# Kernel tuning notes

Hardware: AMD Instinct MI355X
Metric: run time of the kernel (lower is better)

## Reference

```python
import jax, jax.numpy as jnp
import numpy as np

N0, N1, N2, N3 = 524288, 262144, 65536, 8192
E0, E1, E2 = 2621440, 655360, 81920
D_IN, D_H, D_OUT = 256, 256, 64


def setup_inputs() -> dict:
    key = jax.random.key(0)
    ks = jax.random.split(key, 16)
    s = 0.02
    inp = {
        "x": jax.random.normal(ks[0], (N0, D_IN), dtype=jnp.float32),
        "src0": jax.random.randint(ks[1], (E0,), 0, N0, dtype=jnp.int32),
        "dst0": jax.random.randint(ks[2], (E0,), 0, N1, dtype=jnp.int32),
        "src1": jax.random.randint(ks[3], (E1,), 0, N1, dtype=jnp.int32),
        "dst1": jax.random.randint(ks[4], (E1,), 0, N2, dtype=jnp.int32),
        "src2": jax.random.randint(ks[5], (E2,), 0, N2, dtype=jnp.int32),
        "dst2": jax.random.randint(ks[6], (E2,), 0, N3, dtype=jnp.int32),
        "nd0": N1, "nd1": N2, "nd2": N3,
        "Wfc": jax.random.normal(ks[7], (D_IN, D_H), dtype=jnp.float32) * s,
        "bfc": jnp.zeros((D_H,), dtype=jnp.float32),
        "Ws0": jax.random.normal(ks[8], (D_H, D_H), dtype=jnp.float32) * s,
        "Wn0": jax.random.normal(ks[9], (D_H, D_H), dtype=jnp.float32) * s,
        "b0": jnp.zeros((D_H,), dtype=jnp.float32),
        "Ws1": jax.random.normal(ks[10], (D_H, D_H), dtype=jnp.float32) * s,
        "Wn1": jax.random.normal(ks[11], (D_H, D_H), dtype=jnp.float32) * s,
        "b1": jnp.zeros((D_H,), dtype=jnp.float32),
        "Ws2": jax.random.normal(ks[12], (D_H, D_OUT), dtype=jnp.float32) * s,
        "Wn2": jax.random.normal(ks[13], (D_H, D_OUT), dtype=jnp.float32) * s,
        "b2": jnp.zeros((D_OUT,), dtype=jnp.float32),
    }
    return inp


def sage_conv(h, src, dst, n_dst, Ws, Wn, b):
    # DGL SAGEConv 'mean': out = h_dst @ W_self + mean_neigh(h_src) @ W_neigh + b
    h_dst = h[:n_dst]
    msg = jnp.take(h, src, axis=0)                    # [E, d] gather
    agg = jax.ops.segment_sum(msg, dst, num_segments=n_dst)
    cnt = jax.ops.segment_sum(jnp.ones((dst.shape[0],), h.dtype), dst, num_segments=n_dst)
    mean = agg / jnp.maximum(cnt, 1.0)[:, None]
    return h_dst @ Ws + mean @ Wn + b


def reference(x, src0, dst0, src1, dst1, src2, dst2, nd0, nd1, nd2,
              Wfc, bfc, Ws0, Wn0, b0, Ws1, Wn1, b1, Ws2, Wn2, b2):
    h = jax.nn.relu(x @ Wfc + bfc)                    # input projection (dropout=0 -> identity)
    h = jax.nn.relu(sage_conv(h, src0, dst0, nd0, Ws0, Wn0, b0))
    h = jax.nn.relu(sage_conv(h, src1, dst1, nd1, Ws1, Wn1, b1))
    h = sage_conv(h, src2, dst2, nd2, Ws2, Wn2, b2)   # no activation on final layer
    return h
```

## Files before the change

kernel.cpp:

```cpp
#include <hip/hip_runtime.h>

constexpr int N0c = 524288, N1c = 262144, N2c = 65536, N3c = 8192;

typedef __attribute__((ext_vector_type(8))) short   bf16x8;
typedef __attribute__((ext_vector_type(4))) float   f32x4;
typedef __attribute__((ext_vector_type(4))) unsigned short u16x4;

__device__ inline unsigned short f2bf(float f) {
    union { float f; unsigned u; } v; v.f = f;
    unsigned r = v.u + 0x7FFF + ((v.u >> 16) & 1);
    return (unsigned short)(r >> 16);
}
__device__ inline float bf2f(unsigned short u) {
    union { unsigned u; float f; } v; v.u = ((unsigned)u) << 16;
    return v.f;
}

__device__ inline void glds16(const void* g, void* l) {
    __builtin_amdgcn_global_load_lds(
        (const __attribute__((address_space(1))) unsigned int*)g,
        (__attribute__((address_space(3))) unsigned int*)l, 16, 0, 0);
}

__global__ __launch_bounds__(256)
void wconv_k(const float* __restrict__ W, unsigned short* __restrict__ Wt, int K, int N)
{
    const int i = blockIdx.x * 256 + threadIdx.x;
    if (i >= K * N) return;
    const int k = i / N, n = i % N;
    Wt[n * K + k] = f2bf(W[i]);
}

__device__ inline bf16x8 pack_bf8(const float* p) {
    const f32x4 u = *(const f32x4*)p;
    const f32x4 v = *(const f32x4*)(p + 4);
    bf16x8 t;
    #pragma unroll
    for (int j = 0; j < 4; ++j) {
        t[j]     = (short)f2bf(u[j]);
        t[j + 4] = (short)f2bf(v[j]);
    }
    return t;
}

template<int NT, int KC, bool DUAL, bool RELU, bool A_F32, bool OUT_BF16>
__global__ __launch_bounds__(512, 2)
void gemm2(const void* __restrict__ A1v, const void* __restrict__ A2v,
           const unsigned short* __restrict__ Wt1,
           const unsigned short* __restrict__ Wt2,
           const float* __restrict__ bias, void* __restrict__ Cv)
{
    constexpr int N     = NT * 16;
    constexpr int PH    = 256 / KC;
    constexpr int SLOTS = KC / 8;
    constexpr int GPM   = N * SLOTS;
    constexpr int TOTG  = GPM * (DUAL ? 2 : 1);
    static_assert(TOTG == 4096, "LDS sizing");
    __shared__ unsigned short Bs[TOTG * 8];

    const int t    = threadIdx.x;
    const int lane = t & 63;
    const int wv   = t >> 6;
    const int col  = lane & 15;
    const int kg   = lane >> 4;
    const int swz  = (col & 7) << 3;
    const long row0 = (long)blockIdx.x * 128 + wv * 16;

    const unsigned short* A1h = (const unsigned short*)A1v;
    const float*          A1f = (const float*)A1v;
    const unsigned short* A2h = (const unsigned short*)A2v;

    f32x4 acc[NT];
    #pragma unroll
    for (int nt = 0; nt < NT; ++nt) acc[nt] = (f32x4){0.f, 0.f, 0.f, 0.f};

    const long ar = (row0 + col) * 256;

    for (int kh = 0; kh < PH; ++kh) {
        if (kh) __syncthreads();
        #pragma unroll
        for (int it = 0; it < TOTG / 512; ++it) {
            const int g  = it * 512 + t;
            const int m  = DUAL ? (g / GPM) : 0;
            const int gm = DUAL ? (g % GPM) : g;
            const int n  = gm / SLOTS;
            const int s  = gm % SLOTS;
            const int ss = s ^ (n & 7);
            const unsigned short* srcb =
                (m ? Wt2 : Wt1) + n * 256 + kh * KC + ss * 8;
            glds16(srcb, &Bs[(it * 512 + wv * 64) * 8]);
        }
        __syncthreads();

        #pragma unroll
        for (int k0 = 0; k0 < KC; k0 += 32) {
            const int kx = (k0 + kg * 8) ^ swz;
            const long ac = ar + kh * KC + k0 + kg * 8;
            bf16x8 a1, a2;
            if constexpr (A_F32) a1 = pack_bf8(&A1f[ac]);
            else                 a1 = *(const bf16x8*)&A1h[ac];
            if constexpr (DUAL)  a2 = *(const bf16x8*)&A2h[ac];
            #pragma unroll
            for (int nt = 0; nt < NT; ++nt) {
                const bf16x8 b1 = *(const bf16x8*)&Bs[(nt * 16 + col) * KC + kx];
                acc[nt] = __builtin_amdgcn_mfma_f32_16x16x32_bf16(a1, b1, acc[nt], 0, 0, 0);
                if constexpr (DUAL) {
                    const bf16x8 b2 = *(const bf16x8*)&Bs[GPM * 8 + (nt * 16 + col) * KC + kx];
                    acc[nt] = __builtin_amdgcn_mfma_f32_16x16x32_bf16(a2, b2, acc[nt], 0, 0, 0);
                }
            }
        }
    }

    #pragma unroll
    for (int nt = 0; nt < NT; ++nt) {
        const int c = nt * 16 + col;
        const float bb = bias[c];
        #pragma unroll
        for (int rr = 0; rr < 4; ++rr) {
            const long row = row0 + kg * 4 + rr;
            float o = acc[nt][rr] + bb;
            if constexpr (RELU) o = fmaxf(o, 0.f);
            if constexpr (OUT_BF16)
                ((unsigned short*)Cv)[row * N + c] = f2bf(o);
            else
                ((float*)Cv)[row * N + c] = o;
        }
    }
}


__global__ __launch_bounds__(256)
void hist_k(const int* __restrict__ dst, int* __restrict__ hist, int E)
{
    const int i = blockIdx.x * 256 + threadIdx.x;
    if (i < E) atomicAdd(&hist[dst[i]], 1);
}

__global__ __launch_bounds__(256)
void scan1_k(const int* __restrict__ hist, int* __restrict__ offs,
             int* __restrict__ bsum, int n)
{
    __shared__ int sm[256];
    const int t = threadIdx.x;
    const int base = blockIdx.x * 1024 + t * 4;
    int4 v = make_int4(0, 0, 0, 0);
    if (base < n) v = *(const int4*)&hist[base];
    const int s = v.x + v.y + v.z + v.w;
    int val = s;
    sm[t] = val; __syncthreads();
    #pragma unroll
    for (int off = 1; off < 256; off <<= 1) {
        const int add = (t >= off) ? sm[t - off] : 0;
        __syncthreads();
        val += add;
        sm[t] = val;
        __syncthreads();
    }
    const int excl = val - s;
    if (base < n) {
        offs[base]     = excl;
        offs[base + 1] = excl + v.x;
        offs[base + 2] = excl + v.x + v.y;
        offs[base + 3] = excl + v.x + v.y + v.z;
    }
    if (t == 255) bsum[blockIdx.x] = val;
}

__global__ __launch_bounds__(256)
void scan2_k(int* __restrict__ bsum, int nb)
{
    __shared__ int sm[256];
    const int t = threadIdx.x;
    const int s = (t < nb) ? bsum[t] : 0;
    int val = s;
    sm[t] = val; __syncthreads();
    #pragma unroll
    for (int off = 1; off < 256; off <<= 1) {
        const int add = (t >= off) ? sm[t - off] : 0;
        __syncthreads();
        val += add;
        sm[t] = val;
        __syncthreads();
    }
    if (t < nb) bsum[t] = val - s;
}

__global__ __launch_bounds__(256)
void scan3_k(int* __restrict__ offs, const int* __restrict__ bsum)
{
    const int i = blockIdx.x * 256 + threadIdx.x;
    offs[i] += bsum[i >> 10];
}

__global__ __launch_bounds__(256)
void fill_k(const int* __restrict__ src, const int* __restrict__ dst,
            const int* __restrict__ offs, int* __restrict__ hist,
            int* __restrict__ ssrc, int E)
{
    const int i = blockIdx.x * 256 + threadIdx.x;
    if (i < E) {
        const int d = dst[i];
        const int p = atomicAdd(&hist[d], -1) - 1;
        ssrc[offs[d] + p] = src[i];
    }
}

__global__ __launch_bounds__(256)
void agg_k(const unsigned short* __restrict__ h, const int* __restrict__ ssrc,
           const int* __restrict__ offs, unsigned short* __restrict__ agg,
           int n, int E)
{
    const int w    = blockIdx.x * 4 + (threadIdx.x >> 6);
    const int lane = threadIdx.x & 63;
    if (w >= n) return;
    const int beg = offs[w];
    const int end = (w == n - 1) ? E : offs[w + 1];
    float acc[4] = {0.f, 0.f, 0.f, 0.f};
    int j = beg;
    for (; j + 7 < end; j += 8) {
        int s[8];
        #pragma unroll
        for (int q = 0; q < 8; ++q) s[q] = ssrc[j + q];
        u16x4 v[8];
        #pragma unroll
        for (int q = 0; q < 8; ++q)
            v[q] = *(const u16x4*)&h[(size_t)s[q] * 256 + lane * 4];
        #pragma unroll
        for (int q = 0; q < 8; ++q)
            #pragma unroll
            for (int c = 0; c < 4; ++c) acc[c] += bf2f(v[q][c]);
    }
    for (; j < end; ++j) {
        const u16x4 v0 = *(const u16x4*)&h[(size_t)ssrc[j] * 256 + lane * 4];
        #pragma unroll
        for (int c = 0; c < 4; ++c) acc[c] += bf2f(v0[c]);
    }
    const float inv = 1.0f / fmaxf((float)(end - beg), 1.0f);
    u16x4 o;
    #pragma unroll
    for (int c = 0; c < 4; ++c) o[c] = f2bf(acc[c] * inv);
    *(u16x4*)&agg[(size_t)w * 256 + lane * 4] = o;
}

static void build_and_aggregate(const unsigned short* h, const int* src, const int* dst,
                                int n, int E, int* hist, int* offs, int* bsum,
                                int* ssrc, unsigned short* agg, hipStream_t stream)
{
    const dim3 blk(256);
    hipMemsetAsync(hist, 0, (size_t)n * 4, stream);
    hist_k<<<dim3((E + 255) / 256), blk, 0, stream>>>(dst, hist, E);
    scan1_k<<<dim3(n / 1024), blk, 0, stream>>>(hist, offs, bsum, n);
    scan2_k<<<dim3(1), blk, 0, stream>>>(bsum, n / 1024);
    scan3_k<<<dim3(n / 256), blk, 0, stream>>>(offs, bsum);
    fill_k<<<dim3((E + 255) / 256), blk, 0, stream>>>(src, dst, offs, hist, ssrc, E);
    agg_k<<<dim3(n / 4), blk, 0, stream>>>(h, ssrc, offs, agg, n, E);
}

extern "C" void kernel_launch(void* const* d_in, const int* in_sizes, int n_in,
                              void* d_out, int out_size, void* d_ws, size_t ws_size,
                              hipStream_t stream)
{
    const float* x    = (const float*)d_in[0];
    const int*   src0 = (const int*)d_in[1];
    const int*   dst0 = (const int*)d_in[2];
    const int*   src1 = (const int*)d_in[3];
    const int*   dst1 = (const int*)d_in[4];
    const int*   src2 = (const int*)d_in[5];
    const int*   dst2 = (const int*)d_in[6];
    const float* Wfc  = (const float*)d_in[10];
    const float* bfc  = (const float*)d_in[11];
    const float* Ws0  = (const float*)d_in[12];
    const float* Wn0  = (const float*)d_in[13];
    const float* b0   = (const float*)d_in[14];
    const float* Ws1  = (const float*)d_in[15];
    const float* Wn1  = (const float*)d_in[16];
    const float* b1   = (const float*)d_in[17];
    const float* Ws2  = (const float*)d_in[18];
    const float* Wn2  = (const float*)d_in[19];
    const float* b2   = (const float*)d_in[20];
    const int E0 = in_sizes[1], E1 = in_sizes[3], E2 = in_sizes[5];

    char* ws = (char*)d_ws;
    unsigned short* h0   = (unsigned short*)ws;
    unsigned short* h1   = (unsigned short*)(ws + (256ULL << 20));
    unsigned short* h2   = (unsigned short*)(ws + (384ULL << 20));
    unsigned short* agg  = (unsigned short*)(ws + (416ULL << 20));
    unsigned short* Wt   = (unsigned short*)(ws + (544ULL << 20));
    int*            hist = (int*)(ws + (545ULL << 20));
    int*            offs = (int*)(ws + (546ULL << 20));
    int*            bsum = (int*)(ws + (547ULL << 20));
    int*            ssrc = (int*)(ws + (548ULL << 20));

    unsigned short* wfc = Wt;
    unsigned short* ws0 = Wt + 65536;
    unsigned short* wn0 = Wt + 131072;
    unsigned short* ws1 = Wt + 196608;
    unsigned short* wn1 = Wt + 262144;
    unsigned short* ws2 = Wt + 327680;
    unsigned short* wn2 = Wt + 344064;

    const dim3 blk(256);

    wconv_k<<<dim3(256), blk, 0, stream>>>(Wfc, wfc, 256, 256);
    wconv_k<<<dim3(256), blk, 0, stream>>>(Ws0, ws0, 256, 256);
    wconv_k<<<dim3(256), blk, 0, stream>>>(Wn0, wn0, 256, 256);
    wconv_k<<<dim3(256), blk, 0, stream>>>(Ws1, ws1, 256, 256);
    wconv_k<<<dim3(256), blk, 0, stream>>>(Wn1, wn1, 256, 256);
    wconv_k<<<dim3(64),  blk, 0, stream>>>(Ws2, ws2, 256, 64);
    wconv_k<<<dim3(64),  blk, 0, stream>>>(Wn2, wn2, 256, 64);

    gemm2<16, 128, false, true, true, true><<<dim3(N0c / 128), dim3(512), 0, stream>>>(
        x, nullptr, wfc, nullptr, bfc, h0);

    build_and_aggregate(h0, src0, dst0, N1c, E0, hist, offs, bsum, ssrc, agg, stream);
    gemm2<16, 64, true, true, false, true><<<dim3(N1c / 128), dim3(512), 0, stream>>>(
        h0, agg, ws0, wn0, b0, h1);

    build_and_aggregate(h1, src1, dst1, N2c, E1, hist, offs, bsum, ssrc, agg, stream);
    gemm2<16, 64, true, true, false, true><<<dim3(N2c / 128), dim3(512), 0, stream>>>(
        h1, agg, ws1, wn1, b1, h2);

    build_and_aggregate(h2, src2, dst2, N3c, E2, hist, offs, bsum, ssrc, agg, stream);
    gemm2<4, 256, true, false, false, false><<<dim3(N3c / 128), dim3(512), 0, stream>>>(
        h2, agg, ws2, wn2, b2, (float*)d_out);
}
```

Before: 1.020 ms.

## Aggregate four destination rows per wave with interleaved prefetched gathers

Each wavefront now handles four destination rows at once. It keeps one outstanding row gather per destination and round-robins across them, so loads for different rows overlap. This replaces the previous 8-way unrolled batch per row, which left most loads serial for low-degree rows (average degree is about 10 or less). The grid shrinks fourfold, so there are fewer waves. The loop is a data-dependent while with per-row branches, which can cause divergence-like serialization and add register pressure.

```diff
diff --git a/kernel.cpp b/kernel.cpp
--- a/kernel.cpp
+++ b/kernel.cpp
@@ -211,36 +211,55 @@
            const int* __restrict__ offs, unsigned short* __restrict__ agg,
            int n, int E)
 {
-    const int w    = blockIdx.x * 4 + (threadIdx.x >> 6);
+    const int wid  = blockIdx.x * 4 + (threadIdx.x >> 6);
     const int lane = threadIdx.x & 63;
-    if (w >= n) return;
-    const int beg = offs[w];
-    const int end = (w == n - 1) ? E : offs[w + 1];
-    float acc[4] = {0.f, 0.f, 0.f, 0.f};
-    int j = beg;
-    for (; j + 7 < end; j += 8) {
-        int s[8];
-        #pragma unroll
-        for (int q = 0; q < 8; ++q) s[q] = ssrc[j + q];
-        u16x4 v[8];
-        #pragma unroll
-        for (int q = 0; q < 8; ++q)
-            v[q] = *(const u16x4*)&h[(size_t)s[q] * 256 + lane * 4];
-        #pragma unroll
-        for (int q = 0; q < 8; ++q)
+    const int r0   = wid * 4;
+    if (r0 >= n) return;
+
+    int j[4], e[4], deg[4];
+    float acc[4][4];
+    u16x4 v[4];
+    #pragma unroll
+    for (int r = 0; r < 4; ++r) {
+        const int row = r0 + r;
+        j[r] = (row < n) ? offs[row] : 0;
+        e[r] = (row < n) ? ((row == n - 1) ? E : offs[row + 1]) : 0;
+        deg[r] = e[r] - j[r];
+        #pragma unroll
+        for (int c = 0; c < 4; ++c) acc[r][c] = 0.f;
+        if (j[r] < e[r])
+            v[r] = *(const u16x4*)&h[(size_t)ssrc[j[r]] * 256 + lane * 4];
+    }
+
+    bool any = (j[0] < e[0]) | (j[1] < e[1]) | (j[2] < e[2]) | (j[3] < e[3]);
+    while (any) {
+        any = false;
+        #pragma unroll
+        for (int r = 0; r < 4; ++r) {
+            if (j[r] < e[r]) {
+                const u16x4 cur = v[r];
+                const int jn = j[r] + 1;
+                if (jn < e[r])
+                    v[r] = *(const u16x4*)&h[(size_t)ssrc[jn] * 256 + lane * 4];
+                j[r] = jn;
+                #pragma unroll
+                for (int c = 0; c < 4; ++c) acc[r][c] += bf2f(cur[c]);
+                any |= (jn < e[r]);
+            }
+        }
+    }
+
+    #pragma unroll
+    for (int r = 0; r < 4; ++r) {
+        const int row = r0 + r;
+        if (row < n) {
+            const float inv = 1.0f / fmaxf((float)deg[r], 1.0f);
+            u16x4 o;
             #pragma unroll
-            for (int c = 0; c < 4; ++c) acc[c] += bf2f(v[q][c]);
-    }
-    for (; j < end; ++j) {
-        const u16x4 v0 = *(const u16x4*)&h[(size_t)ssrc[j] * 256 + lane * 4];
-        #pragma unroll
-        for (int c = 0; c < 4; ++c) acc[c] += bf2f(v0[c]);
-    }
-    const float inv = 1.0f / fmaxf((float)(end - beg), 1.0f);
-    u16x4 o;
-    #pragma unroll
-    for (int c = 0; c < 4; ++c) o[c] = f2bf(acc[c] * inv);
-    *(u16x4*)&agg[(size_t)w * 256 + lane * 4] = o;
+            for (int c = 0; c < 4; ++c) o[c] = f2bf(acc[r][c] * inv);
+            *(u16x4*)&agg[(size_t)row * 256 + lane * 4] = o;
+        }
+    }
 }
 
 static void build_and_aggregate(const unsigned short* h, const int* src, const int* dst,
@@ -254,7 +273,7 @@
     scan2_k<<<dim3(1), blk, 0, stream>>>(bsum, n / 1024);
     scan3_k<<<dim3(n / 256), blk, 0, stream>>>(offs, bsum);
     fill_k<<<dim3((E + 255) / 256), blk, 0, stream>>>(src, dst, offs, hist, ssrc, E);
-    agg_k<<<dim3(n / 4), blk, 0, stream>>>(h, ssrc, offs, agg, n, E);
+    agg_k<<<dim3(n / 16), blk, 0, stream>>>(h, ssrc, offs, agg, n, E);
 }
 
 extern "C" void kernel_launch(void* const* d_in, const int* in_sizes, int n_in,
```

Result: slower. 1.218 ms (+19.5%).
